# Performance work log

Hardware: AMD Instinct MI355X
Metric: run time of the kernel (lower is better)

Reference implementation:

```python
import jax, jax.numpy as jnp
import numpy as np
import math

B, H, S, D = 2, 16, 2048, 128
CONTEXT = 2048

def setup_inputs() -> dict:
    key = jax.random.key(0)
    kq, kk, kt = jax.random.split(key, 3)
    q = jax.random.normal(kq, (B, H, S, D), dtype=jnp.float32)
    k = jax.random.normal(kk, (B, H, S, D), dtype=jnp.float32)
    # head_scales init: torch.linspace(1.2, 1.2, H) -> constant 1.2
    head_scales = jnp.full((H,), 1.2, dtype=jnp.float32)
    # ALiBi slopes: 2 ** (-8 * i / H) for i in 1..H
    slopes = (2.0 ** (-8.0 * jnp.arange(1, H + 1, dtype=jnp.float32) / H)).astype(jnp.float32)
    positions = jnp.arange(CONTEXT, dtype=jnp.float32)
    token_indices = jnp.sort(jax.random.randint(kt, (B, S), 0, CONTEXT), axis=-1)
    return {"q": q, "k": k, "head_scales": head_scales, "slopes": slopes,
            "positions": positions, "token_indices": token_indices}

def reference(q, k, head_scales, slopes, positions, token_indices):
    head_dim = q.shape[-1]
    base_scale = 1.0 / math.sqrt(head_dim)
    # before_scores: per-head scaling of q
    q_scaled = q * (head_scales[None, :, None, None] * base_scale)
    # attention scores [B, H, S, S]
    scores = jnp.einsum('bhqd,bhkd->bhqk', q_scaled, k)
    # compute_after: ALiBi bias from gathered positions
    pos = positions[token_indices]                      # [B, S]
    pos_diff = pos[:, :, None] - pos[:, None, :]        # [B, S, S]
    bias = slopes[None, :, None, None] * pos_diff[:, None, :, :]  # [B, H, S, S]
    return scores - bias
```

## Files before the change

### kernel.cpp

```cpp
#include <hip/hip_runtime.h>
#include <hip/hip_bf16.h>

#define S 2048
#define D 128
#define NH 16
#define TM 128
#define TN 128
#define BK 64
#define LROW (BK + 8)

typedef __bf16 bf16x8 __attribute__((ext_vector_type(8)));
typedef __bf16 bf16x4 __attribute__((ext_vector_type(4)));
typedef float  f32x4  __attribute__((ext_vector_type(4)));

__global__ __launch_bounds__(256, 4)
void alibi_scores(const float* __restrict__ q,
                  const float* __restrict__ k,
                  const float* __restrict__ head_scales,
                  const float* __restrict__ slopes,
                  const float* __restrict__ positions,
                  const int* __restrict__ tok,
                  float* __restrict__ out)
{
    __shared__ __align__(16) __bf16 As[TM * LROW];
    __shared__ __align__(16) __bf16 Bs[TN * LROW];
    __shared__ float posQ[TM];
    __shared__ float posK[TN];

    const int tid = threadIdx.x;

    const int wgid = blockIdx.x + (blockIdx.y << 4) + (blockIdx.z << 8);
    const int lin  = ((wgid & 7) << 10) | (wgid >> 3);
    const int bh   = lin >> 8;
    const int b    = bh >> 4;
    const int h    = bh & 15;
    const int tm   = ((lin >> 4) & 15) * TM;
    const int tn   = (lin & 15) * TN;

    if (tid < TM)
        posQ[tid] = positions[tok[b * S + tm + tid]];
    else
        posK[tid - TM] = positions[tok[b * S + tn + (tid - TM)]];

    const float* qb = q + (size_t)bh * S * D;
    const float* kb = k + (size_t)bh * S * D;

    const int lane = tid & 63;
    const int wv   = tid >> 6;
    const int wm   = (wv >> 1) * 64;
    const int wn   = (wv & 1) * 64;
    const int col  = lane & 15;
    const int quad = lane >> 4;

    f32x4 acc[4][4];
    #pragma unroll
    for (int i = 0; i < 4; ++i)
        #pragma unroll
        for (int j = 0; j < 4; ++j)
            acc[i][j] = (f32x4){0.f, 0.f, 0.f, 0.f};

    #pragma unroll
    for (int kc = 0; kc < D; kc += BK) {
        #pragma unroll
        for (int it = 0; it < 8; ++it) {
            const int g = it * 256 + tid;
            const int r = g >> 4;
            const int c = (g & 15) * 4;
            f32x4 va = *reinterpret_cast<const f32x4*>(qb + (size_t)(tm + r) * D + kc + c);
            f32x4 vb = *reinterpret_cast<const f32x4*>(kb + (size_t)(tn + r) * D + kc + c);
            bf16x4 a4, b4;
            #pragma unroll
            for (int j = 0; j < 4; ++j) { a4[j] = (__bf16)va[j]; b4[j] = (__bf16)vb[j]; }
            *reinterpret_cast<bf16x4*>(&As[r * LROW + c]) = a4;
            *reinterpret_cast<bf16x4*>(&Bs[r * LROW + c]) = b4;
        }
        __syncthreads();

        #pragma unroll
        for (int ks = 0; ks < BK; ks += 32) {
            const int kf = ks + quad * 8;
            bf16x8 af[4], bfr[4];
            #pragma unroll
            for (int mi = 0; mi < 4; ++mi)
                af[mi] = *reinterpret_cast<const bf16x8*>(&As[(wm + mi * 16 + col) * LROW + kf]);
            #pragma unroll
            for (int ni = 0; ni < 4; ++ni)
                bfr[ni] = *reinterpret_cast<const bf16x8*>(&Bs[(wn + ni * 16 + col) * LROW + kf]);
            #pragma unroll
            for (int mi = 0; mi < 4; ++mi)
                #pragma unroll
                for (int ni = 0; ni < 4; ++ni)
                    acc[mi][ni] = __builtin_amdgcn_mfma_f32_16x16x32_bf16(
                        bfr[ni], af[mi], acc[mi][ni], 0, 0, 0);
        }
        __syncthreads();
    }

    const float scale = head_scales[h] * 0.08838834764831845f;
    const float slope = slopes[h];
    float* ob = out + (size_t)bh * S * S;

    #pragma unroll
    for (int mi = 0; mi < 4; ++mi) {
        const int qr = wm + mi * 16 + col;
        const float sp = slope * posQ[qr];
        float* orow = ob + (size_t)(tm + qr) * S + tn;
        #pragma unroll
        for (int ni = 0; ni < 4; ++ni) {
            const int kc0 = wn + ni * 16 + quad * 4;
            const f32x4 pk = *reinterpret_cast<const f32x4*>(&posK[kc0]);
            f32x4 v;
            #pragma unroll
            for (int r = 0; r < 4; ++r)
                v[r] = acc[mi][ni][r] * scale + (slope * pk[r] - sp);
            __builtin_nontemporal_store(v, reinterpret_cast<f32x4*>(orow + kc0));
        }
    }
}

extern "C" void kernel_launch(void* const* d_in, const int* in_sizes, int n_in,
                              void* d_out, int out_size, void* d_ws, size_t ws_size,
                              hipStream_t stream)
{
    (void)in_sizes; (void)n_in; (void)d_ws; (void)ws_size; (void)out_size;
    const float* q  = (const float*)d_in[0];
    const float* k  = (const float*)d_in[1];
    const float* hs = (const float*)d_in[2];
    const float* sl = (const float*)d_in[3];
    const float* ps = (const float*)d_in[4];
    const int*   ti = (const int*)d_in[5];
    float* out      = (float*)d_out;

    dim3 grid(S / TN, S / TM, 2 * NH);
    alibi_scores<<<grid, 256, 0, stream>>>(q, k, hs, sl, ps, ti, out);
}
```

Measured before the change: 707.5 us.

## Load MFMA operands directly from global memory, removing LDS staging and barriers

Each wave now reads its q and k fragments straight from global memory into registers, converting to bf16 in place, so the shared-memory tiles and __syncthreads are gone. Token positions are gathered per thread into registers instead of shared arrays. The output stores become ordinary stores instead of nontemporal ones, and launch bounds drop to 2 blocks per CU. This removes LDS traffic and barrier stalls, but each q/k row is now read by both waves that share it rather than once per block. It also relies on cache for reuse, and the loads are strided per lane.

```diff
diff --git a/kernel.cpp b/kernel.cpp
--- a/kernel.cpp
+++ b/kernel.cpp
@@ -6,14 +6,12 @@
 #define NH 16
 #define TM 128
 #define TN 128
-#define BK 64
-#define LROW (BK + 8)
 
 typedef __bf16 bf16x8 __attribute__((ext_vector_type(8)));
-typedef __bf16 bf16x4 __attribute__((ext_vector_type(4)));
 typedef float  f32x4  __attribute__((ext_vector_type(4)));
+typedef int    i32x4  __attribute__((ext_vector_type(4)));
 
-__global__ __launch_bounds__(256, 4)
+__global__ __launch_bounds__(256, 2)
 void alibi_scores(const float* __restrict__ q,
                   const float* __restrict__ k,
                   const float* __restrict__ head_scales,
@@ -22,11 +20,6 @@
                   const int* __restrict__ tok,
                   float* __restrict__ out)
 {
-    __shared__ __align__(16) __bf16 As[TM * LROW];
-    __shared__ __align__(16) __bf16 Bs[TN * LROW];
-    __shared__ float posQ[TM];
-    __shared__ float posK[TN];
-
     const int tid = threadIdx.x;
 
     const int wgid = blockIdx.x + (blockIdx.y << 4) + (blockIdx.z << 8);
@@ -37,20 +30,30 @@
     const int tm   = ((lin >> 4) & 15) * TM;
     const int tn   = (lin & 15) * TN;
 
-    if (tid < TM)
-        posQ[tid] = positions[tok[b * S + tm + tid]];
-    else
-        posK[tid - TM] = positions[tok[b * S + tn + (tid - TM)]];
-
-    const float* qb = q + (size_t)bh * S * D;
-    const float* kb = k + (size_t)bh * S * D;
-
     const int lane = tid & 63;
     const int wv   = tid >> 6;
-    const int wm   = (wv >> 1) * 64;
-    const int wn   = (wv & 1) * 64;
+    const int wr   = (wv >> 1) * 64;
+    const int wc   = (wv & 1) * 64;
     const int col  = lane & 15;
     const int quad = lane >> 4;
+
+    const float* qrow = q + ((size_t)bh * S + (tm + wr + col)) * D + quad * 8;
+    const float* krow = k + ((size_t)bh * S + (tn + wc + col)) * D + quad * 8;
+
+    float pq[4];
+    f32x4 pk4[4];
+    {
+        const int* tq = tok + b * S + tm + wr + col;
+        const int* tk = tok + b * S + tn + wc + quad * 4;
+        #pragma unroll
+        for (int mi = 0; mi < 4; ++mi) pq[mi] = positions[tq[mi * 16]];
+        #pragma unroll
+        for (int ni = 0; ni < 4; ++ni) {
+            i32x4 t4 = *reinterpret_cast<const i32x4*>(tk + ni * 16);
+            #pragma unroll
+            for (int r = 0; r < 4; ++r) pk4[ni][r] = positions[t4[r]];
+        }
+    }
 
     f32x4 acc[4][4];
     #pragma unroll
@@ -60,40 +63,34 @@
             acc[i][j] = (f32x4){0.f, 0.f, 0.f, 0.f};
 
     #pragma unroll
-    for (int kc = 0; kc < D; kc += BK) {
+    for (int ks = 0; ks < 4; ++ks) {
+        bf16x8 qf[4], kf[4];
         #pragma unroll
-        for (int it = 0; it < 8; ++it) {
-            const int g = it * 256 + tid;
-            const int r = g >> 4;
-            const int c = (g & 15) * 4;
-            f32x4 va = *reinterpret_cast<const f32x4*>(qb + (size_t)(tm + r) * D + kc + c);
-            f32x4 vb = *reinterpret_cast<const f32x4*>(kb + (size_t)(tn + r) * D + kc + c);
-            bf16x4 a4, b4;
+        for (int mi = 0; mi < 4; ++mi) {
+            f32x4 lo = *reinterpret_cast<const f32x4*>(qrow + mi * 16 * D + ks * 32);
+            f32x4 hi = *reinterpret_cast<const f32x4*>(qrow + mi * 16 * D + ks * 32 + 4);
             #pragma unroll
-            for (int j = 0; j < 4; ++j) { a4[j] = (__bf16)va[j]; b4[j] = (__bf16)vb[j]; }
-            *reinterpret_cast<bf16x4*>(&As[r * LROW + c]) = a4;
-            *reinterpret_cast<bf16x4*>(&Bs[r * LROW + c]) = b4;
+            for (int j = 0; j < 4; ++j) {
+                qf[mi][j]     = (__bf16)lo[j];
+                qf[mi][j + 4] = (__bf16)hi[j];
+            }
         }
-        __syncthreads();
-
         #pragma unroll
-        for (int ks = 0; ks < BK; ks += 32) {
-            const int kf = ks + quad * 8;
-            bf16x8 af[4], bfr[4];
+        for (int ni = 0; ni < 4; ++ni) {
+            f32x4 lo = *reinterpret_cast<const f32x4*>(krow + ni * 16 * D + ks * 32);
+            f32x4 hi = *reinterpret_cast<const f32x4*>(krow + ni * 16 * D + ks * 32 + 4);
             #pragma unroll
-            for (int mi = 0; mi < 4; ++mi)
-                af[mi] = *reinterpret_cast<const bf16x8*>(&As[(wm + mi * 16 + col) * LROW + kf]);
+            for (int j = 0; j < 4; ++j) {
+                kf[ni][j]     = (__bf16)lo[j];
+                kf[ni][j + 4] = (__bf16)hi[j];
+            }
+        }
+        #pragma unroll
+        for (int mi = 0; mi < 4; ++mi)
             #pragma unroll
             for (int ni = 0; ni < 4; ++ni)
-                bfr[ni] = *reinterpret_cast<const bf16x8*>(&Bs[(wn + ni * 16 + col) * LROW + kf]);
-            #pragma unroll
-            for (int mi = 0; mi < 4; ++mi)
-                #pragma unroll
-                for (int ni = 0; ni < 4; ++ni)
-                    acc[mi][ni] = __builtin_amdgcn_mfma_f32_16x16x32_bf16(
-                        bfr[ni], af[mi], acc[mi][ni], 0, 0, 0);
-        }
-        __syncthreads();
+                acc[mi][ni] = __builtin_amdgcn_mfma_f32_16x16x32_bf16(
+                    kf[ni], qf[mi], acc[mi][ni], 0, 0, 0);
     }
 
     const float scale = head_scales[h] * 0.08838834764831845f;
@@ -102,18 +99,15 @@
 
     #pragma unroll
     for (int mi = 0; mi < 4; ++mi) {
-        const int qr = wm + mi * 16 + col;
-        const float sp = slope * posQ[qr];
-        float* orow = ob + (size_t)(tm + qr) * S + tn;
+        const float sp = slope * pq[mi];
+        float* orow = ob + (size_t)(tm + wr + mi * 16 + col) * S + tn + wc;
         #pragma unroll
         for (int ni = 0; ni < 4; ++ni) {
-            const int kc0 = wn + ni * 16 + quad * 4;
-            const f32x4 pk = *reinterpret_cast<const f32x4*>(&posK[kc0]);
             f32x4 v;
             #pragma unroll
             for (int r = 0; r < 4; ++r)
-                v[r] = acc[mi][ni][r] * scale + (slope * pk[r] - sp);
-            __builtin_nontemporal_store(v, reinterpret_cast<f32x4*>(orow + kc0));
+                v[r] = acc[mi][ni][r] * scale + (slope * pk4[ni][r] - sp);
+            *reinterpret_cast<f32x4*>(orow + ni * 16 + quad * 4) = v;
         }
     }
 }
```

Result: slower. 777.3 us (+9.9%).
